# Kernel tuning notes

Measured on AMD Instinct MI355X. Metric: run time of the kernel, lower is better.

## Reference

```python
import jax, jax.numpy as jnp
import numpy as np


def chamfer_bidirectional(p1, p2):
    """p1: [B,N,3], p2: [B,M,3]. Returns (min_sq_dist1 [B,N], min_sq_dist2 [B,M])."""
    # squared pairwise distances via ||a||^2 + ||b||^2 - 2 a.b  (avoids [B,N,M,3] diff tensor)
    n1 = jnp.sum(p1 * p1, axis=-1)          # [B,N]
    n2 = jnp.sum(p2 * p2, axis=-1)          # [B,M]
    cross = jnp.einsum('bnd,bmd->bnm', p1, p2)  # [B,N,M]
    d = n1[:, :, None] + n2[:, None, :] - 2.0 * cross  # [B,N,M]
    d = jnp.maximum(d, 0.0)
    return jnp.min(d, axis=2), jnp.min(d, axis=1)


def setup_inputs() -> dict:
    key = jax.random.key(0)
    k1, k2, k3, k4, k5 = jax.random.split(key, 5)
    B = 8
    return {
        'pred': jax.random.normal(k1, (B, 10, 3), dtype=jnp.float32),
        'target': jax.random.normal(k2, (B, 10, 3), dtype=jnp.float32),
        'coarse': jax.random.normal(k3, (B, 3, 1024), dtype=jnp.float32),
        'fine': jax.random.normal(k4, (B, 3, 4096), dtype=jnp.float32),
        'gt_pc': jax.random.normal(k5, (B, 4096, 3), dtype=jnp.float32),
    }


def reference(pred, target, coarse, fine, gt_pc):
    kp_loss = jnp.mean((pred - target) ** 2)
    c1, c2 = chamfer_bidirectional(jnp.transpose(coarse, (0, 2, 1)), gt_pc)
    f1, f2 = chamfer_bidirectional(jnp.transpose(fine, (0, 2, 1)), gt_pc)
    coarse_loss = jnp.mean(c1) + jnp.mean(c2)
    fine_loss = jnp.mean(f1) + jnp.mean(f2)
    return kp_loss + coarse_loss + fine_loss
```

## Files before the change

kernel.cpp:

```cpp
#include <hip/hip_runtime.h>
#include <math.h>

#define BTILE 1024
#define SPLIT 8
#define APB   32
#define SEG   128

template<bool A_PLANAR, bool B_PLANAR>
__device__ __forceinline__ void chamfer_block(
    const float* __restrict__ A, int An,
    const float* __restrict__ B, int Bn,
    int lbid, float scale,
    float (&sb)[4][BTILE], float (&red)[256],
    float* __restrict__ wslot)
{
    const int bpb   = An / APB;
    const int batch = lbid / bpb;
    const int ablk  = lbid % bpb;
    const float* __restrict__ Ab = A + (size_t)batch * 3 * An;
    const float* __restrict__ Bb = B + (size_t)batch * 3 * Bn;

    const int tid = threadIdx.x;
    const int al  = tid & (APB - 1);
    const int sp  = tid >> 5;
    const int p   = ablk * APB + al;

    float ax, ay, az;
    if (A_PLANAR) { ax = Ab[p];     ay = Ab[An + p];  az = Ab[2*An + p]; }
    else          { ax = Ab[3*p];   ay = Ab[3*p + 1]; az = Ab[3*p + 2];  }
    const float a2 = fmaf(ax, ax, fmaf(ay, ay, az * az));

    float m0 = 3.402823466e38f, m1 = m0, m2 = m0, m3 = m0;

    const int NT = Bn / BTILE;
    for (int t = 0; t < NT; ++t) {
        const int t0 = t * BTILE;
        for (int k = tid; k < BTILE; k += 256) {
            float x, y, z;
            if (B_PLANAR) {
                x = Bb[t0 + k]; y = Bb[Bn + t0 + k]; z = Bb[2*Bn + t0 + k];
            } else {
                int base = 3 * (t0 + k);
                x = Bb[base]; y = Bb[base + 1]; z = Bb[base + 2];
            }
            sb[0][k] = -2.0f * x;
            sb[1][k] = -2.0f * y;
            sb[2][k] = -2.0f * z;
            sb[3][k] = fmaf(x, x, fmaf(y, y, z * z));
        }
        __syncthreads();

        const float4* __restrict__ px = (const float4*)&sb[0][sp * SEG];
        const float4* __restrict__ py = (const float4*)&sb[1][sp * SEG];
        const float4* __restrict__ pz = (const float4*)&sb[2][sp * SEG];
        const float4* __restrict__ pw = (const float4*)&sb[3][sp * SEG];
#pragma unroll 8
        for (int g = 0; g < SEG / 4; ++g) {
            float4 x = px[g], y = py[g], z = pz[g], w = pw[g];
            m0 = fminf(m0, fmaf(ax, x.x, fmaf(ay, y.x, fmaf(az, z.x, w.x))));
            m1 = fminf(m1, fmaf(ax, x.y, fmaf(ay, y.y, fmaf(az, z.y, w.y))));
            m2 = fminf(m2, fmaf(ax, x.z, fmaf(ay, y.z, fmaf(az, z.z, w.z))));
            m3 = fminf(m3, fmaf(ax, x.w, fmaf(ay, y.w, fmaf(az, z.w, w.w))));
        }
        __syncthreads();
    }
    float best = fminf(fminf(m0, m1), fminf(m2, m3));

    red[tid] = best;
    __syncthreads();
#pragma unroll
    for (int s = 128; s >= APB; s >>= 1) {
        if (tid < s) red[tid] = fminf(red[tid], red[tid + s]);
        __syncthreads();
    }

    if (tid < APB) {
        float d = fmaxf(0.0f, a2 + red[tid]) * scale;
#pragma unroll
        for (int off = APB / 2; off > 0; off >>= 1) d += __shfl_down(d, off, APB);
        if (tid == 0) *wslot = d;
    }
}

__device__ __forceinline__ void kp_block(const float* __restrict__ a,
                                         const float* __restrict__ b, int n,
                                         float (&red)[256], float* __restrict__ wslot)
{
    int tid = threadIdx.x;
    float s = 0.0f;
    for (int i = tid; i < n; i += 256) {
        float d = a[i] - b[i];
        s = fmaf(d, d, s);
    }
    for (int off = 32; off > 0; off >>= 1) s += __shfl_down(s, off, 64);
    if ((tid & 63) == 0) red[tid >> 6] = s;
    __syncthreads();
    if (tid == 0) *wslot = (red[0] + red[1] + red[2] + red[3]) / (float)n;
}

__global__ __launch_bounds__(256) void fused_all(
    const float* __restrict__ pred, const float* __restrict__ target, int nkp,
    const float* __restrict__ coarse, int Nc,
    const float* __restrict__ fine, int Nf,
    const float* __restrict__ gt, int M,
    int r1, int r2, int r3, int r4,
    float sc_f1, float sc_f2, float sc_c2, float sc_c1,
    float* __restrict__ ws)
{
    __shared__ __align__(16) float sb[4][BTILE];
    __shared__ float red[256];
    const int bid = blockIdx.x;
    float* wslot = ws + bid;

    if (bid < r1)
        chamfer_block<true,  false>(fine,   Nf, gt,     M,  bid,      sc_f1, sb, red, wslot);
    else if (bid < r2)
        chamfer_block<false, true >(gt,     M,  fine,   Nf, bid - r1, sc_f2, sb, red, wslot);
    else if (bid < r3)
        chamfer_block<false, true >(gt,     M,  coarse, Nc, bid - r2, sc_c2, sb, red, wslot);
    else if (bid < r4)
        chamfer_block<true,  false>(coarse, Nc, gt,     M,  bid - r3, sc_c1, sb, red, wslot);
    else
        kp_block(pred, target, nkp, red, wslot);
}

__global__ __launch_bounds__(256) void finalize(const float* __restrict__ ws, int n,
                                                float* __restrict__ out)
{
    int tid = threadIdx.x;
    float s = 0.0f;
    for (int i = tid; i < n; i += 256) s += ws[i];
    for (int off = 32; off > 0; off >>= 1) s += __shfl_down(s, off, 64);
    __shared__ float r[4];
    if ((tid & 63) == 0) r[tid >> 6] = s;
    __syncthreads();
    if (tid == 0) out[0] = r[0] + r[1] + r[2] + r[3];
}

extern "C" void kernel_launch(void* const* d_in, const int* in_sizes, int n_in,
                              void* d_out, int out_size, void* d_ws, size_t ws_size,
                              hipStream_t stream) {
    const float* pred   = (const float*)d_in[0];
    const float* target = (const float*)d_in[1];
    const float* coarse = (const float*)d_in[2];
    const float* fine   = (const float*)d_in[3];
    const float* gt     = (const float*)d_in[4];
    float* out = (float*)d_out;
    float* ws  = (float*)d_ws;

    const int nkp = in_sizes[0];
    const int B   = nkp / 30;
    const int Nc  = in_sizes[2] / (3 * B);
    const int Nf  = in_sizes[3] / (3 * B);
    const int M   = in_sizes[4] / (3 * B);

    const int nb_f1 = B * (Nf / APB);
    const int nb_f2 = B * (M  / APB);
    const int nb_c2 = B * (M  / APB);
    const int nb_c1 = B * (Nc / APB);
    const int r1 = nb_f1;
    const int r2 = r1 + nb_f2;
    const int r3 = r2 + nb_c2;
    const int r4 = r3 + nb_c1;
    const int nb = r4 + 1;

    fused_all<<<nb, 256, 0, stream>>>(
        pred, target, nkp, coarse, Nc, fine, Nf, gt, M,
        r1, r2, r3, r4,
        1.0f / (B * Nf), 1.0f / (B * M), 1.0f / (B * M), 1.0f / (B * Nc),
        ws);
    finalize<<<1, 256, 0, stream>>>(ws, nb, out);
}
```

Measured before the change: 112.4 us.

## Process two A points per thread and fuse final reduction via atomics

Each thread now evaluates two A points against every staged B point, so each shared-memory read of B feeds twice as many FMAs and the number of blocks halves. The separate finalize kernel is replaced by per-block atomicAdd into a workspace accumulator, with a last-block counter that writes the output, plus a memset. Block order for the coarse segments is swapped and launch bounds request 8 blocks per CU. The trade-offs are more registers per thread, fewer blocks for latency hiding, and a float atomic accumulation whose summation order is nondeterministic.

```diff
diff --git a/kernel.cpp b/kernel.cpp
--- a/kernel.cpp
+++ b/kernel.cpp
@@ -2,35 +2,40 @@
 #include <math.h>
 
 #define BTILE 1024
-#define SPLIT 8
-#define APB   32
 #define SEG   128
 
 template<bool A_PLANAR, bool B_PLANAR>
-__device__ __forceinline__ void chamfer_block(
+__device__ __forceinline__ float chamfer_block(
     const float* __restrict__ A, int An,
     const float* __restrict__ B, int Bn,
     int lbid, float scale,
-    float (&sb)[4][BTILE], float (&red)[256],
-    float* __restrict__ wslot)
+    float (&sb)[4][BTILE], float (&red)[512])
 {
-    const int bpb   = An / APB;
+    const int bpb   = An >> 6;
     const int batch = lbid / bpb;
     const int ablk  = lbid % bpb;
     const float* __restrict__ Ab = A + (size_t)batch * 3 * An;
     const float* __restrict__ Bb = B + (size_t)batch * 3 * Bn;
 
-    const int tid = threadIdx.x;
-    const int al  = tid & (APB - 1);
-    const int sp  = tid >> 5;
-    const int p   = ablk * APB + al;
+    const int tid  = threadIdx.x;
+    const int slot = tid & 31;
+    const int sp   = tid >> 5;
+    const int p0   = ablk * 64 + slot;
+    const int p1   = p0 + 32;
 
-    float ax, ay, az;
-    if (A_PLANAR) { ax = Ab[p];     ay = Ab[An + p];  az = Ab[2*An + p]; }
-    else          { ax = Ab[3*p];   ay = Ab[3*p + 1]; az = Ab[3*p + 2];  }
-    const float a2 = fmaf(ax, ax, fmaf(ay, ay, az * az));
+    float a0x, a0y, a0z, a1x, a1y, a1z;
+    if (A_PLANAR) {
+        a0x = Ab[p0];   a0y = Ab[An + p0];   a0z = Ab[2*An + p0];
+        a1x = Ab[p1];   a1y = Ab[An + p1];   a1z = Ab[2*An + p1];
+    } else {
+        a0x = Ab[3*p0]; a0y = Ab[3*p0 + 1];  a0z = Ab[3*p0 + 2];
+        a1x = Ab[3*p1]; a1y = Ab[3*p1 + 1];  a1z = Ab[3*p1 + 2];
+    }
+    const float a0s = fmaf(a0x, a0x, fmaf(a0y, a0y, a0z * a0z));
+    const float a1s = fmaf(a1x, a1x, fmaf(a1y, a1y, a1z * a1z));
 
-    float m0 = 3.402823466e38f, m1 = m0, m2 = m0, m3 = m0;
+    const float BIG = 3.402823466e38f;
+    float n00 = BIG, n01 = BIG, n10 = BIG, n11 = BIG;
 
     const int NT = Bn / BTILE;
     for (int t = 0; t < NT; ++t) {
@@ -54,37 +59,52 @@
         const float4* __restrict__ py = (const float4*)&sb[1][sp * SEG];
         const float4* __restrict__ pz = (const float4*)&sb[2][sp * SEG];
         const float4* __restrict__ pw = (const float4*)&sb[3][sp * SEG];
-#pragma unroll 8
+#pragma unroll 2
         for (int g = 0; g < SEG / 4; ++g) {
             float4 x = px[g], y = py[g], z = pz[g], w = pw[g];
-            m0 = fminf(m0, fmaf(ax, x.x, fmaf(ay, y.x, fmaf(az, z.x, w.x))));
-            m1 = fminf(m1, fmaf(ax, x.y, fmaf(ay, y.y, fmaf(az, z.y, w.y))));
-            m2 = fminf(m2, fmaf(ax, x.z, fmaf(ay, y.z, fmaf(az, z.z, w.z))));
-            m3 = fminf(m3, fmaf(ax, x.w, fmaf(ay, y.w, fmaf(az, z.w, w.w))));
+            float d0, d1, d2, d3;
+            d0 = fmaf(a0x, x.x, fmaf(a0y, y.x, fmaf(a0z, z.x, w.x)));
+            d1 = fmaf(a0x, x.y, fmaf(a0y, y.y, fmaf(a0z, z.y, w.y)));
+            d2 = fmaf(a0x, x.z, fmaf(a0y, y.z, fmaf(a0z, z.z, w.z)));
+            d3 = fmaf(a0x, x.w, fmaf(a0y, y.w, fmaf(a0z, z.w, w.w)));
+            n00 = fminf(fminf(d0, d1), n00);
+            n01 = fminf(fminf(d2, d3), n01);
+            d0 = fmaf(a1x, x.x, fmaf(a1y, y.x, fmaf(a1z, z.x, w.x)));
+            d1 = fmaf(a1x, x.y, fmaf(a1y, y.y, fmaf(a1z, z.y, w.y)));
+            d2 = fmaf(a1x, x.z, fmaf(a1y, y.z, fmaf(a1z, z.z, w.z)));
+            d3 = fmaf(a1x, x.w, fmaf(a1y, y.w, fmaf(a1z, z.w, w.w)));
+            n10 = fminf(fminf(d0, d1), n10);
+            n11 = fminf(fminf(d2, d3), n11);
         }
         __syncthreads();
     }
-    float best = fminf(fminf(m0, m1), fminf(m2, m3));
 
-    red[tid] = best;
+    red[sp * 32 + slot]       = fminf(n00, n01);
+    red[256 + sp * 32 + slot] = fminf(n10, n11);
     __syncthreads();
 #pragma unroll
-    for (int s = 128; s >= APB; s >>= 1) {
-        if (tid < s) red[tid] = fminf(red[tid], red[tid + s]);
+    for (int st = 4; st > 0; st >>= 1) {
+        if (sp < st) {
+            red[sp*32 + slot]       = fminf(red[sp*32 + slot],       red[(sp+st)*32 + slot]);
+            red[256 + sp*32 + slot] = fminf(red[256 + sp*32 + slot], red[256 + (sp+st)*32 + slot]);
+        }
         __syncthreads();
     }
 
-    if (tid < APB) {
-        float d = fmaxf(0.0f, a2 + red[tid]) * scale;
+    float contrib = 0.0f;
+    if (tid < 32) {
+        float d = fmaxf(0.0f, a0s + red[slot]) + fmaxf(0.0f, a1s + red[256 + slot]);
+        d *= scale;
 #pragma unroll
-        for (int off = APB / 2; off > 0; off >>= 1) d += __shfl_down(d, off, APB);
-        if (tid == 0) *wslot = d;
+        for (int off = 16; off > 0; off >>= 1) d += __shfl_down(d, off, 32);
+        contrib = d;
     }
+    return contrib;
 }
 
-__device__ __forceinline__ void kp_block(const float* __restrict__ a,
-                                         const float* __restrict__ b, int n,
-                                         float (&red)[256], float* __restrict__ wslot)
+__device__ __forceinline__ float kp_block(const float* __restrict__ a,
+                                          const float* __restrict__ b, int n,
+                                          float (&red)[512])
 {
     int tid = threadIdx.x;
     float s = 0.0f;
@@ -95,46 +115,46 @@
     for (int off = 32; off > 0; off >>= 1) s += __shfl_down(s, off, 64);
     if ((tid & 63) == 0) red[tid >> 6] = s;
     __syncthreads();
-    if (tid == 0) *wslot = (red[0] + red[1] + red[2] + red[3]) / (float)n;
+    float r = 0.0f;
+    if (tid == 0) r = (red[0] + red[1] + red[2] + red[3]) / (float)n;
+    return r;
 }
 
-__global__ __launch_bounds__(256) void fused_all(
+__global__ __launch_bounds__(256, 8) void fused_all(
     const float* __restrict__ pred, const float* __restrict__ target, int nkp,
     const float* __restrict__ coarse, int Nc,
     const float* __restrict__ fine, int Nf,
     const float* __restrict__ gt, int M,
     int r1, int r2, int r3, int r4,
-    float sc_f1, float sc_f2, float sc_c2, float sc_c1,
-    float* __restrict__ ws)
+    float sc_f1, float sc_f2, float sc_c1, float sc_c2,
+    float* __restrict__ ws, float* __restrict__ out)
 {
     __shared__ __align__(16) float sb[4][BTILE];
-    __shared__ float red[256];
+    __shared__ float red[512];
     const int bid = blockIdx.x;
-    float* wslot = ws + bid;
+    const int nb  = gridDim.x;
 
+    float contrib;
     if (bid < r1)
-        chamfer_block<true,  false>(fine,   Nf, gt,     M,  bid,      sc_f1, sb, red, wslot);
+        contrib = chamfer_block<true,  false>(fine,   Nf, gt,     M,  bid,      sc_f1, sb, red);
     else if (bid < r2)
-        chamfer_block<false, true >(gt,     M,  fine,   Nf, bid - r1, sc_f2, sb, red, wslot);
+        contrib = chamfer_block<false, true >(gt,     M,  fine,   Nf, bid - r1, sc_f2, sb, red);
     else if (bid < r3)
-        chamfer_block<false, true >(gt,     M,  coarse, Nc, bid - r2, sc_c2, sb, red, wslot);
+        contrib = chamfer_block<true,  false>(coarse, Nc, gt,     M,  bid - r2, sc_c1, sb, red);
     else if (bid < r4)
-        chamfer_block<true,  false>(coarse, Nc, gt,     M,  bid - r3, sc_c1, sb, red, wslot);
+        contrib = chamfer_block<false, true >(gt,     M,  coarse, Nc, bid - r3, sc_c2, sb, red);
     else
-        kp_block(pred, target, nkp, red, wslot);
-}
+        contrib = kp_block(pred, target, nkp, red);
 
-__global__ __launch_bounds__(256) void finalize(const float* __restrict__ ws, int n,
-                                                float* __restrict__ out)
-{
-    int tid = threadIdx.x;
-    float s = 0.0f;
-    for (int i = tid; i < n; i += 256) s += ws[i];
-    for (int off = 32; off > 0; off >>= 1) s += __shfl_down(s, off, 64);
-    __shared__ float r[4];
-    if ((tid & 63) == 0) r[tid >> 6] = s;
-    __syncthreads();
-    if (tid == 0) out[0] = r[0] + r[1] + r[2] + r[3];
+    if (threadIdx.x == 0) {
+        atomicAdd(ws, contrib);
+        __threadfence();
+        unsigned old = atomicAdd((unsigned*)ws + 4, 1u);
+        if (old == (unsigned)(nb - 1)) {
+            __threadfence();
+            out[0] = atomicAdd(ws, 0.0f);
+        }
+    }
 }
 
 extern "C" void kernel_launch(void* const* d_in, const int* in_sizes, int n_in,
@@ -154,20 +174,20 @@
     const int Nf  = in_sizes[3] / (3 * B);
     const int M   = in_sizes[4] / (3 * B);
 
-    const int nb_f1 = B * (Nf / APB);
-    const int nb_f2 = B * (M  / APB);
-    const int nb_c2 = B * (M  / APB);
-    const int nb_c1 = B * (Nc / APB);
+    const int nb_f1 = B * (Nf / 64);
+    const int nb_f2 = B * (M  / 64);
+    const int nb_c1 = B * (Nc / 64);
+    const int nb_c2 = B * (M  / 64);
     const int r1 = nb_f1;
     const int r2 = r1 + nb_f2;
-    const int r3 = r2 + nb_c2;
-    const int r4 = r3 + nb_c1;
+    const int r3 = r2 + nb_c1;
+    const int r4 = r3 + nb_c2;
     const int nb = r4 + 1;
 
+    hipMemsetAsync(ws, 0, 64, stream);
     fused_all<<<nb, 256, 0, stream>>>(
         pred, target, nkp, coarse, Nc, fine, Nf, gt, M,
         r1, r2, r3, r4,
-        1.0f / (B * Nf), 1.0f / (B * M), 1.0f / (B * M), 1.0f / (B * Nc),
-        ws);
-    finalize<<<1, 256, 0, stream>>>(ws, nb, out);
+        1.0f / (B * Nf), 1.0f / (B * M), 1.0f / (B * Nc), 1.0f / (B * M),
+        ws, out);
 }
```

Result: slower. 124.1 us (+10.4%).
